# Performance work log

Hardware: AMD Instinct MI355X
Metric: run time of the kernel (lower is better)

The kernel has to match this reference:

```python
import jax, jax.numpy as jnp
import numpy as np

B, N, C, H = 16, 577, 768, 12
KEEP_RATE = 0.7


def setup_inputs() -> dict:
    key = jax.random.key(0)
    k1, k2, k3 = jax.random.split(key, 3)
    x = jax.random.normal(k1, (B, N, C), dtype=jnp.float32)
    W_qkv = jax.random.normal(k2, (C, 3 * C), dtype=jnp.float32) * 0.02
    W_proj = jax.random.normal(k3, (C, C), dtype=jnp.float32) * 0.02
    b_proj = jnp.zeros((C,), dtype=jnp.float32)
    return {"x": x, "W_qkv": W_qkv, "W_proj": W_proj, "b_proj": b_proj}


def reference(x, W_qkv, W_proj, b_proj):
    b, n, c = x.shape
    h = H
    dh = c // h
    scale = dh ** (-0.5)

    # qkv projection -> q,k,v each [B,H,N,dh]
    qkv = (x @ W_qkv).reshape(b, n, 3, h, dh)
    qkv = jnp.transpose(qkv, (2, 0, 3, 1, 4))
    q, k, v = qkv[0], qkv[1], qkv[2]

    # full attention scores [B,H,N,N] (materialized, as in the source)
    attn = jnp.einsum('bhnd,bhmd->bhnm', q, k) * scale

    # --- top_pool from row-0 (CLS) scores, attn_method == 'SUM_ABS_1' ---
    # attn[:, :, 0, :] -> [B,H,N]; sum |.| over heads -> [B,N] (== mean over C=1 channel)
    attn_weight = jnp.sum(jnp.abs(attn[:, :, 0, :]), axis=1)  # [B,N]
    # exclude_first=True: drop CLS, topk over remaining N-1, alpha1=1, alpha2=0 (C==1 -> std=0)
    w = attn_weight[:, 1:]                       # [B, N-1]
    keep_num = max(int((n - 1) * KEEP_RATE), 1)  # static
    _, idx = jax.lax.top_k(w, keep_num)          # [B, keep_num]
    idx = jnp.sort(idx, axis=1)
    idx = jnp.concatenate(
        [jnp.zeros((b, 1), dtype=idx.dtype), idx + 1], axis=1)  # prepend CLS index 0
    # expand to [B, keep_num+1, dim] as in torch (pool dim kwarg == self.dim)
    keep_index = jnp.broadcast_to(idx[:, :, None], (b, keep_num + 1, c))

    # standard attention output
    a = jax.nn.softmax(attn, axis=-1)
    out = jnp.einsum('bhnm,bhmd->bhnd', a, v)    # [B,H,N,dh]
    out = jnp.transpose(out, (0, 2, 1, 3)).reshape(b, n, c)
    out = out @ W_proj + b_proj
    return out, keep_index
```

## Files before the change

kernel.cpp:

```cpp
#include <hip/hip_runtime.h>
#include <hip/hip_bf16.h>
#include <stdint.h>

#define B_    16
#define N_    577
#define C_    768
#define H_    12
#define M_    (B_*N_)
#define QKVN  (3*C_)
#define NKEEP 403
#define KROWS (NKEEP+1)
#define VTLD  640
#define PTLD  72

typedef short s16x8 __attribute__((ext_vector_type(8)));
typedef float f32x4 __attribute__((ext_vector_type(4)));

__device__ __forceinline__ unsigned short f2bf(float x){
  unsigned int u = __float_as_uint(x);
  u += 0x7FFF + ((u >> 16) & 1);
  return (unsigned short)(u >> 16);
}

__device__ __forceinline__ void gld_lds16(const void* g, void* l){
  __builtin_amdgcn_global_load_lds(
      (const __attribute__((address_space(1))) unsigned int*)g,
      (__attribute__((address_space(3))) unsigned int*)l, 16, 0, 0);
}

template<int NT>
__device__ __forceinline__ void tile_map(int L, int& mt, int& nt){
  constexpr int NB = 73*NT;
  int x = L & 7, j = L >> 3;
  if(j < 9*NT){
    nt = j/9; mt = x*9 + (j - nt*9);
  } else {
    mt = 72;
    int offt = 0;
    #pragma unroll
    for(int y=0;y<8;y++) if(y<x) offt += ((NB-1-y)>>3) + 1 - 9*NT;
    nt = offt + (j - 9*NT);
  }
}

__global__ void k_cvt_x(const float* __restrict__ x, unsigned short* __restrict__ xb){
  int i = blockIdx.x*256 + threadIdx.x;
  float4 v = ((const float4*)x)[i];
  ushort4 o; o.x=f2bf(v.x); o.y=f2bf(v.y); o.z=f2bf(v.z); o.w=f2bf(v.w);
  ((ushort4*)xb)[i] = o;
}

__global__ void k_transpose_cvt(const float* __restrict__ in, unsigned short* __restrict__ out,
                                int R, int CC){
  __shared__ float tile[64][65];
  int r0 = blockIdx.y*64, c0 = blockIdx.x*64;
  int tx = threadIdx.x & 63, ty = threadIdx.x >> 6;
  #pragma unroll
  for(int i=0;i<16;i++){
    int r = ty + i*4;
    tile[r][tx] = in[(size_t)(r0+r)*CC + c0 + tx];
  }
  __syncthreads();
  #pragma unroll
  for(int i=0;i<16;i++){
    int c = ty + i*4;
    out[(size_t)(c0+c)*R + r0 + tx] = f2bf(tile[tx][c]);
  }
}

template<int LDC_, bool BF16OUT, bool FUSEV, int NT>
__global__ __launch_bounds__(256) void k_gemm_bt(const unsigned short* __restrict__ A,
                          const unsigned short* __restrict__ Bt,
                          void* __restrict__ Cout,
                          const float* __restrict__ bias, int Mdim,
                          unsigned short* __restrict__ vtbuf){
  __shared__ __align__(16) unsigned short As[128*32];
  __shared__ __align__(16) unsigned short Bs[128*32];
  const int t = threadIdx.x;
  const int w = t>>6, l = t&63, lq = l>>4, lr = l&15;
  const int wm = w>>1, wn = w&1;
  int mt, nt; tile_map<NT>(blockIdx.x, mt, nt);
  const int m0 = mt*128, n0 = nt*128;
  int rA0 = m0 + (t>>2);       if(rA0 >= Mdim) rA0 = Mdim-1;
  int rA1 = m0 + ((t+256)>>2); if(rA1 >= Mdim) rA1 = Mdim-1;
  const unsigned short* gA0 = A  + (size_t)rA0*768 + (t&3)*8;
  const unsigned short* gA1 = A  + (size_t)rA1*768 + (t&3)*8;
  const unsigned short* gB0 = Bt + (size_t)(n0 + (t>>2))*768 + (t&3)*8;
  const unsigned short* gB1 = Bt + (size_t)(n0 + ((t+256)>>2))*768 + (t&3)*8;
  unsigned short* lA0 = As + (size_t)w*512;
  unsigned short* lA1 = As + 2048 + (size_t)w*512;
  unsigned short* lB0 = Bs + (size_t)w*512;
  unsigned short* lB1 = Bs + 2048 + (size_t)w*512;
  f32x4 acc[4][4] = {};
  for(int kt=0; kt<24; ++kt){
    __syncthreads();
    gld_lds16(gA0, lA0); gld_lds16(gA1, lA1);
    gld_lds16(gB0, lB0); gld_lds16(gB1, lB1);
    gA0 += 32; gA1 += 32; gB0 += 32; gB1 += 32;
    __syncthreads();
    s16x8 af[4], bfr[4];
    #pragma unroll
    for(int it=0;it<4;it++) af[it]  = *(const s16x8*)&As[(wm*64+it*16+lr)*32 + lq*8];
    #pragma unroll
    for(int jt=0;jt<4;jt++) bfr[jt] = *(const s16x8*)&Bs[(wn*64+jt*16+lr)*32 + lq*8];
    #pragma unroll
    for(int it=0;it<4;it++)
      #pragma unroll
      for(int jt=0;jt<4;jt++)
        acc[it][jt] = __builtin_amdgcn_mfma_f32_16x16x32_bf16(af[it], bfr[jt], acc[it][jt], 0,0,0);
  }
  if(FUSEV && n0 >= 1536){
    #pragma unroll
    for(int it=0;it<4;it++){
      int tok0 = m0 + wm*64 + it*16 + lq*4;
      #pragma unroll
      for(int jt=0;jt<4;jt++){
        int vrow = (n0 - 1536) + wn*64 + jt*16 + lr;
        ushort4 pk; unsigned short* pks = (unsigned short*)&pk;
        #pragma unroll
        for(int r=0;r<4;r++) pks[r] = f2bf(acc[it][jt][r]);
        int b0 = tok0/577, t0 = tok0 - b0*577;
        if(tok0 + 3 < M_ && t0 + 3 < 577){
          *(ushort4*)&vtbuf[(size_t)(b0*768 + vrow)*VTLD + t0] = pk;
        } else {
          #pragma unroll
          for(int r=0;r<4;r++){
            int tg = tok0 + r;
            if(tg < M_){
              int bb = tg/577, tt = tg - bb*577;
              vtbuf[(size_t)(bb*768 + vrow)*VTLD + tt] = pks[r];
            }
          }
        }
      }
    }
  } else {
    #pragma unroll
    for(int it=0;it<4;it++){
      #pragma unroll
      for(int r=0;r<4;r++){
        int row = m0 + wm*64 + it*16 + lq*4 + r;
        if(row < Mdim){
          #pragma unroll
          for(int jt=0;jt<4;jt++){
            int col = n0 + wn*64 + jt*16 + lr;
            float v = acc[it][jt][r];
            if constexpr (BF16OUT)
              ((unsigned short*)Cout)[(size_t)row*LDC_ + col] = f2bf(v);
            else
              ((float*)Cout)[(size_t)row*LDC_ + col] = v + bias[col];
          }
        }
      }
    }
  }
}

__global__ __launch_bounds__(256,4) void k_attn(const unsigned short* __restrict__ qkv,
                                                const unsigned short* __restrict__ vtbuf,
                                                unsigned short* __restrict__ aout){
  __shared__ __align__(16) unsigned short Ks[64*64];
  __shared__ __align__(16) unsigned short Vt[64*64];
  __shared__ __align__(16) unsigned short Ptt[128*PTLD];
  __shared__ float Ls[4][2][16][4];
  const int blk = blockIdx.x;
  const int bh = blk % 192, qt = blk / 192;
  const int b = bh / 12, h = bh % 12;
  const int t = threadIdx.x, w = t>>6, l = t&63, lq = l>>4, lr = l&15;
  const size_t base = (size_t)(b*577)*2304 + h*64;
  const int q0 = qt*128;
  s16x8 bq[2][2];
  #pragma unroll
  for(int it=0;it<2;it++){
    int qrow = q0 + w*32 + it*16 + lr; if(qrow > 576) qrow = 576;
    #pragma unroll
    for(int ks=0;ks<2;ks++)
      bq[it][ks] = *(const s16x8*)&qkv[base + (size_t)qrow*2304 + ks*32 + lq*8];
  }
  const int srow = w*8 + (l>>3);
  const int cswz8 = (((l&7) ^ (l>>3)) << 3);
  unsigned short* ldsK = Ks + (size_t)w*512;
  unsigned short* ldsV = Vt + (size_t)w*512;
  const unsigned short* gVbase = vtbuf + (size_t)(bh*64)*VTLD + cswz8;

  f32x4 acc_o[2][4] = {};
  float lsum[2] = {0.f, 0.f};
  const float CEXP = 0.18033688011112043f;

  for(int j0=0; j0<577; j0+=64){
    __syncthreads();
    #pragma unroll
    for(int i=0;i<2;i++){
      int krow = j0 + i*32 + srow; if(krow > 576) krow = 576;
      gld_lds16(qkv + base + 768 + (size_t)krow*2304 + cswz8, ldsK + i*2048);
      gld_lds16(gVbase + (size_t)(i*32 + srow)*VTLD + j0,     ldsV + i*2048);
    }
    __syncthreads();
    f32x4 accs[2][4] = {};
    #pragma unroll
    for(int ks=0;ks<2;ks++){
      s16x8 ak[4];
      #pragma unroll
      for(int jt=0;jt<4;jt++){
        int j = jt*16 + lr;
        ak[jt] = *(const s16x8*)&Ks[j*64 + (((4*ks+lq) ^ (j&7))<<3)];
      }
      #pragma unroll
      for(int it=0;it<2;it++)
        #pragma unroll
        for(int jt=0;jt<4;jt++)
          accs[it][jt] = __builtin_amdgcn_mfma_f32_16x16x32_bf16(ak[jt], bq[it][ks], accs[it][jt], 0,0,0);
    }
    #pragma unroll
    for(int it=0;it<2;it++){
      int qlocal = w*32 + it*16 + lr;
      #pragma unroll
      for(int jt=0;jt<4;jt++){
        ushort4 pk;
        unsigned short* pks = (unsigned short*)&pk;
        #pragma unroll
        for(int r=0;r<4;r++){
          int j = j0 + jt*16 + lq*4 + r;
          float p = exp2f(accs[it][jt][r] * CEXP);
          if(j > 576) p = 0.f;
          lsum[it] += p;
          pks[r] = f2bf(p);
        }
        *(ushort4*)&Ptt[qlocal*PTLD + jt*16 + lq*4] = pk;
      }
    }
    #pragma unroll
    for(int ks=0;ks<2;ks++){
      s16x8 ap[2], bv[4];
      #pragma unroll
      for(int it=0;it<2;it++)
        ap[it] = *(const s16x8*)&Ptt[(w*32+it*16+lr)*PTLD + ks*32 + lq*8];
      #pragma unroll
      for(int dt=0;dt<4;dt++){
        int d = dt*16 + lr;
        bv[dt] = *(const s16x8*)&Vt[d*64 + (((4*ks+lq) ^ (d&7))<<3)];
      }
      #pragma unroll
      for(int it=0;it<2;it++)
        #pragma unroll
        for(int dt=0;dt<4;dt++)
          acc_o[it][dt] = __builtin_amdgcn_mfma_f32_16x16x32_bf16(ap[it], bv[dt], acc_o[it][dt], 0,0,0);
    }
  }
  #pragma unroll
  for(int it=0;it<2;it++) Ls[w][it][lr][lq] = lsum[it];
  #pragma unroll
  for(int it=0;it<2;it++){
    #pragma unroll
    for(int r=0;r<4;r++){
      int n = q0 + w*32 + it*16 + lq*4 + r;
      if(n <= 576){
        int q16 = lq*4 + r;
        float lt = Ls[w][it][q16][0] + Ls[w][it][q16][1] + Ls[w][it][q16][2] + Ls[w][it][q16][3];
        float inv = 1.f / lt;
        #pragma unroll
        for(int dt=0;dt<4;dt++)
          aout[(size_t)(b*577+n)*768 + h*64 + dt*16 + lr] = f2bf(acc_o[it][dt][r]*inv);
      }
    }
  }
}

__global__ void k_qcls(const float* __restrict__ x, const float* __restrict__ Wqkv,
                       float* __restrict__ qcls){
  __shared__ float xs[768];
  __shared__ float part[4][64];
  const int b = blockIdx.y, j0 = blockIdx.x*64;
  const int t = threadIdx.x;
  const float* xr = x + (size_t)b*577*768;
  xs[t] = xr[t]; xs[t+256] = xr[t+256]; xs[t+512] = xr[t+512];
  __syncthreads();
  const int jl = t & 63, cs = t >> 6;
  float acc = 0.f;
  const float* wp = Wqkv + (size_t)(cs*192)*2304 + j0 + jl;
  #pragma unroll 4
  for(int c=0;c<192;c++){ acc += xs[cs*192+c] * wp[0]; wp += 2304; }
  part[cs][jl] = acc;
  __syncthreads();
  if(t < 64) qcls[b*768 + j0 + t] = part[0][t]+part[1][t]+part[2][t]+part[3][t];
}
__global__ void k_u(const float* __restrict__ Wqkv, const float* __restrict__ qcls,
                    float* __restrict__ u){
  int h = blockIdx.x, b = blockIdx.y, c = threadIdx.x;
  const float* qc = qcls + b*768 + h*64;
  const float* wr = Wqkv + (size_t)c*2304 + 768 + h*64;
  float acc = 0.f;
  #pragma unroll
  for(int d=0;d<64;d++) acc += wr[d]*qc[d];
  u[(size_t)(b*12+h)*768 + c] = acc;
}
__global__ void k_attw(const float* __restrict__ x, const float* __restrict__ u,
                       float* __restrict__ attw){
  int blk = blockIdx.x;
  int b = blk/577, m = blk%577;
  int lane = threadIdx.x;
  const float* xr = x + (size_t)(b*577+m)*768;
  const float* ub = u + (size_t)b*12*768;
  float part[12];
  #pragma unroll
  for(int h=0;h<12;h++) part[h]=0.f;
  #pragma unroll
  for(int i=0;i<12;i++){
    float xv = xr[i*64 + lane];
    #pragma unroll
    for(int h=0;h<12;h++) part[h] += xv * ub[h*768 + i*64 + lane];
  }
  float s = 0.f;
  #pragma unroll
  for(int h=0;h<12;h++){
    float v = part[h];
    #pragma unroll
    for(int off=32; off; off>>=1) v += __shfl_xor(v, off);
    s += fabsf(v);
  }
  if(lane==0) attw[b*577 + m] = 0.125f * s;
}
__global__ void k_topk(const float* __restrict__ attw, int* __restrict__ idxbuf){
  __shared__ float sw[576];
  __shared__ int wtot[9];
  int b = blockIdx.x, t = threadIdx.x;
  float wv = attw[b*577 + 1 + t];
  sw[t] = wv;
  __syncthreads();
  int rank = 0;
  for(int j=0;j<576;j++){
    float wj = sw[j];
    rank += (wj > wv) || (wj == wv && j < t);
  }
  bool kept = rank < NKEEP;
  unsigned long long mask = __ballot(kept);
  int wid = t>>6, lane = t&63;
  int pos = __popcll(mask & ((1ull<<lane)-1ull));
  if(lane==0) wtot[wid] = __popcll(mask);
  __syncthreads();
  int off0 = 0;
  for(int q=0;q<wid;q++) off0 += wtot[q];
  if(kept) idxbuf[b*KROWS + 1 + off0 + pos] = t+1;
  if(t==0) idxbuf[b*KROWS] = 0;
}
__global__ void k_fill_keep(const int* __restrict__ idxbuf, float* __restrict__ out2){
  int i4 = blockIdx.x*256 + threadIdx.x;
  float v = (float)idxbuf[i4/192];
  ((float4*)out2)[i4] = make_float4(v,v,v,v);
}

extern "C" void kernel_launch(void* const* d_in, const int* in_sizes, int n_in,
                              void* d_out, int out_size, void* d_ws, size_t ws_size,
                              hipStream_t stream){
  const float* x     = (const float*)d_in[0];
  const float* Wqkv  = (const float*)d_in[1];
  const float* Wproj = (const float*)d_in[2];
  const float* bias  = (const float*)d_in[3];
  float* out  = (float*)d_out;
  float* out2 = out + (size_t)M_*768;

  char* ws = (char*)d_ws;
  size_t off = 0;
  auto alloc = [&](size_t bytes)->void*{ void* p = ws + off; off += (bytes + 255) & ~(size_t)255; return p; };
  unsigned short* xb     = (unsigned short*)alloc((size_t)M_*768*2);
  unsigned short* wqkvT  = (unsigned short*)alloc((size_t)QKVN*768*2);
  unsigned short* wprojT = (unsigned short*)alloc((size_t)768*768*2);
  unsigned short* qkvb   = (unsigned short*)alloc((size_t)M_*QKVN*2);
  unsigned short* aoutb  = (unsigned short*)alloc((size_t)M_*768*2);
  unsigned short* vtbuf  = (unsigned short*)alloc((size_t)192*64*VTLD*2);
  float* qcls   = (float*)alloc((size_t)16*768*4);
  float* u      = (float*)alloc((size_t)16*12*768*4);
  float* attw   = (float*)alloc((size_t)16*577*4);
  int*   idxbuf = (int*)alloc((size_t)16*KROWS*4);

  k_cvt_x<<<6924, 256, 0, stream>>>(x, xb);
  k_transpose_cvt<<<dim3(36,12), 256, 0, stream>>>(Wqkv,  wqkvT, 768, 2304);
  k_transpose_cvt<<<dim3(12,12), 256, 0, stream>>>(Wproj, wprojT, 768, 768);
  k_gemm_bt<QKVN, true, true, 18><<<73*18, 256, 0, stream>>>(xb, wqkvT, qkvb, nullptr, M_, vtbuf);
  k_qcls<<<dim3(12,16), 256, 0, stream>>>(x, Wqkv, qcls);
  k_u<<<dim3(12,16), 768, 0, stream>>>(Wqkv, qcls, u);
  k_attw<<<16*577, 64, 0, stream>>>(x, u, attw);
  k_topk<<<16, 576, 0, stream>>>(attw, idxbuf);
  k_fill_keep<<<(16*KROWS*768/4 + 255)/256, 256, 0, stream>>>(idxbuf, out2);
  k_attn<<<960, 256, 0, stream>>>(qkvb, vtbuf, aoutb);
  k_gemm_bt<768, false, false, 6><<<73*6, 256, 0, stream>>>(aoutb, wprojT, out, bias, M_, nullptr);
}
```

Measured before the change: 284.5 us.

## Double-buffer LDS tiles in GEMM and attention to overlap loads with MFMA

Both the bf16 GEMM and the attention kernel now use two LDS stages. The next K-slice (GEMM) or K/V tile (attention) is issued into the alternate buffer before computing on the current one, which also drops one barrier per iteration. The aim is to hide global-to-LDS latency behind MFMA work. The cost is doubled LDS per block: the attention kernel rises to roughly 50 KB, which may cut the number of resident blocks per CU below the four its launch bounds target. Correctness also depends on the async LDS loads having completed before each barrier.

```diff
diff --git a/kernel.cpp b/kernel.cpp
--- a/kernel.cpp
+++ b/kernel.cpp
@@ -74,8 +74,8 @@
                           void* __restrict__ Cout,
                           const float* __restrict__ bias, int Mdim,
                           unsigned short* __restrict__ vtbuf){
-  __shared__ __align__(16) unsigned short As[128*32];
-  __shared__ __align__(16) unsigned short Bs[128*32];
+  __shared__ __align__(16) unsigned short As[2*128*32];
+  __shared__ __align__(16) unsigned short Bs[2*128*32];
   const int t = threadIdx.x;
   const int w = t>>6, l = t&63, lq = l>>4, lr = l&15;
   const int wm = w>>1, wn = w&1;
@@ -87,28 +87,39 @@
   const unsigned short* gA1 = A  + (size_t)rA1*768 + (t&3)*8;
   const unsigned short* gB0 = Bt + (size_t)(n0 + (t>>2))*768 + (t&3)*8;
   const unsigned short* gB1 = Bt + (size_t)(n0 + ((t+256)>>2))*768 + (t&3)*8;
-  unsigned short* lA0 = As + (size_t)w*512;
-  unsigned short* lA1 = As + 2048 + (size_t)w*512;
-  unsigned short* lB0 = Bs + (size_t)w*512;
-  unsigned short* lB1 = Bs + 2048 + (size_t)w*512;
   f32x4 acc[4][4] = {};
-  for(int kt=0; kt<24; ++kt){
-    __syncthreads();
-    gld_lds16(gA0, lA0); gld_lds16(gA1, lA1);
-    gld_lds16(gB0, lB0); gld_lds16(gB1, lB1);
-    gA0 += 32; gA1 += 32; gB0 += 32; gB1 += 32;
-    __syncthreads();
+
+  auto issue = [&](int kt, int s){
+    const int ko = kt*32;
+    unsigned short* a = As + s*4096 + w*512;
+    unsigned short* b = Bs + s*4096 + w*512;
+    gld_lds16(gA0 + ko, a);
+    gld_lds16(gA1 + ko, a + 2048);
+    gld_lds16(gB0 + ko, b);
+    gld_lds16(gB1 + ko, b + 2048);
+  };
+  auto compute = [&](int s){
     s16x8 af[4], bfr[4];
     #pragma unroll
-    for(int it=0;it<4;it++) af[it]  = *(const s16x8*)&As[(wm*64+it*16+lr)*32 + lq*8];
-    #pragma unroll
-    for(int jt=0;jt<4;jt++) bfr[jt] = *(const s16x8*)&Bs[(wn*64+jt*16+lr)*32 + lq*8];
+    for(int it=0;it<4;it++) af[it]  = *(const s16x8*)&As[s*4096 + (wm*64+it*16+lr)*32 + lq*8];
+    #pragma unroll
+    for(int jt=0;jt<4;jt++) bfr[jt] = *(const s16x8*)&Bs[s*4096 + (wn*64+jt*16+lr)*32 + lq*8];
     #pragma unroll
     for(int it=0;it<4;it++)
       #pragma unroll
       for(int jt=0;jt<4;jt++)
         acc[it][jt] = __builtin_amdgcn_mfma_f32_16x16x32_bf16(af[it], bfr[jt], acc[it][jt], 0,0,0);
-  }
+  };
+
+  issue(0, 0);
+  for(int kt=1; kt<24; ++kt){
+    __syncthreads();
+    issue(kt, kt&1);
+    compute((kt-1)&1);
+  }
+  __syncthreads();
+  compute(1);
+
   if(FUSEV && n0 >= 1536){
     #pragma unroll
     for(int it=0;it<4;it++){
@@ -159,8 +170,8 @@
 __global__ __launch_bounds__(256,4) void k_attn(const unsigned short* __restrict__ qkv,
                                                 const unsigned short* __restrict__ vtbuf,
                                                 unsigned short* __restrict__ aout){
-  __shared__ __align__(16) unsigned short Ks[64*64];
-  __shared__ __align__(16) unsigned short Vt[64*64];
+  __shared__ __align__(16) unsigned short Ks[2*64*64];
+  __shared__ __align__(16) unsigned short Vt[2*64*64];
   __shared__ __align__(16) unsigned short Ptt[128*PTLD];
   __shared__ float Ls[4][2][16][4];
   const int blk = blockIdx.x;
@@ -179,23 +190,26 @@
   }
   const int srow = w*8 + (l>>3);
   const int cswz8 = (((l&7) ^ (l>>3)) << 3);
-  unsigned short* ldsK = Ks + (size_t)w*512;
-  unsigned short* ldsV = Vt + (size_t)w*512;
   const unsigned short* gVbase = vtbuf + (size_t)(bh*64)*VTLD + cswz8;
 
   f32x4 acc_o[2][4] = {};
   float lsum[2] = {0.f, 0.f};
   const float CEXP = 0.18033688011112043f;
 
-  for(int j0=0; j0<577; j0+=64){
-    __syncthreads();
+  auto issueKV = [&](int j0, int s){
     #pragma unroll
     for(int i=0;i<2;i++){
       int krow = j0 + i*32 + srow; if(krow > 576) krow = 576;
-      gld_lds16(qkv + base + 768 + (size_t)krow*2304 + cswz8, ldsK + i*2048);
-      gld_lds16(gVbase + (size_t)(i*32 + srow)*VTLD + j0,     ldsV + i*2048);
-    }
+      gld_lds16(qkv + base + 768 + (size_t)krow*2304 + cswz8, Ks + s*4096 + w*512 + i*2048);
+      gld_lds16(gVbase + (size_t)(i*32 + srow)*VTLD + j0,     Vt + s*4096 + w*512 + i*2048);
+    }
+  };
+
+  issueKV(0, 0);
+  for(int jt5=0; jt5<10; ++jt5){
+    const int j0 = jt5*64, s = jt5&1;
     __syncthreads();
+    if(jt5 < 9) issueKV(j0+64, s^1);
     f32x4 accs[2][4] = {};
     #pragma unroll
     for(int ks=0;ks<2;ks++){
@@ -203,7 +217,7 @@
       #pragma unroll
       for(int jt=0;jt<4;jt++){
         int j = jt*16 + lr;
-        ak[jt] = *(const s16x8*)&Ks[j*64 + (((4*ks+lq) ^ (j&7))<<3)];
+        ak[jt] = *(const s16x8*)&Ks[s*4096 + j*64 + (((4*ks+lq) ^ (j&7))<<3)];
       }
       #pragma unroll
       for(int it=0;it<2;it++)
@@ -238,7 +252,7 @@
       #pragma unroll
       for(int dt=0;dt<4;dt++){
         int d = dt*16 + lr;
-        bv[dt] = *(const s16x8*)&Vt[d*64 + (((4*ks+lq) ^ (d&7))<<3)];
+        bv[dt] = *(const s16x8*)&Vt[s*4096 + d*64 + (((4*ks+lq) ^ (d&7))<<3)];
       }
       #pragma unroll
       for(int it=0;it<2;it++)
```

Result: slower. 296.3 us (+4.2%).

## Use 64-row tiles for output projection and peel attention edge tile

Applied to the files above, without the earlier changes.

Adds a separate projection GEMM kernel with 64x128 tiles, so it launches 870 blocks instead of 438 and fills more compute units. The tile mapping is generalized to handle the last M tiles. The attention key loop is split into full tiles plus one masked edge tile, which removes the per-element bounds check from the main loop. GEMM addressing now uses a per-iteration offset instead of pointer increments. Smaller tiles raise the B-matrix reload traffic.

```diff
diff --git a/kernel.cpp b/kernel.cpp
--- a/kernel.cpp
+++ b/kernel.cpp
@@ -28,18 +28,19 @@
       (__attribute__((address_space(3))) unsigned int*)l, 16, 0, 0);
 }
 
-template<int NT>
+template<int NT, int M9, int MTILES>
 __device__ __forceinline__ void tile_map(int L, int& mt, int& nt){
-  constexpr int NB = 73*NT;
+  constexpr int NB = MTILES*NT;
   int x = L & 7, j = L >> 3;
-  if(j < 9*NT){
-    nt = j/9; mt = x*9 + (j - nt*9);
+  if(j < M9*NT){
+    nt = j/M9; mt = x*M9 + (j - nt*M9);
   } else {
-    mt = 72;
     int offt = 0;
     #pragma unroll
-    for(int y=0;y<8;y++) if(y<x) offt += ((NB-1-y)>>3) + 1 - 9*NT;
-    nt = offt + (j - 9*NT);
+    for(int y=0;y<8;y++) if(y<x) offt += ((NB-1-y)>>3) + 1 - M9*NT;
+    int ft = offt + (j - M9*NT);
+    mt = 8*M9 + ft/NT;
+    nt = ft - (ft/NT)*NT;
   }
 }
 
@@ -79,7 +80,7 @@
   const int t = threadIdx.x;
   const int w = t>>6, l = t&63, lq = l>>4, lr = l&15;
   const int wm = w>>1, wn = w&1;
-  int mt, nt; tile_map<NT>(blockIdx.x, mt, nt);
+  int mt, nt; tile_map<NT, 9, 73>(blockIdx.x, mt, nt);
   const int m0 = mt*128, n0 = nt*128;
   int rA0 = m0 + (t>>2);       if(rA0 >= Mdim) rA0 = Mdim-1;
   int rA1 = m0 + ((t+256)>>2); if(rA1 >= Mdim) rA1 = Mdim-1;
@@ -93,10 +94,10 @@
   unsigned short* lB1 = Bs + 2048 + (size_t)w*512;
   f32x4 acc[4][4] = {};
   for(int kt=0; kt<24; ++kt){
-    __syncthreads();
-    gld_lds16(gA0, lA0); gld_lds16(gA1, lA1);
-    gld_lds16(gB0, lB0); gld_lds16(gB1, lB1);
-    gA0 += 32; gA1 += 32; gB0 += 32; gB1 += 32;
+    const int ko = kt*32;
+    __syncthreads();
+    gld_lds16(gA0 + ko, lA0); gld_lds16(gA1 + ko, lA1);
+    gld_lds16(gB0 + ko, lB0); gld_lds16(gB1 + ko, lB1);
     __syncthreads();
     s16x8 af[4], bfr[4];
     #pragma unroll
@@ -156,6 +157,58 @@
   }
 }
 
+__global__ __launch_bounds__(256) void k_gemm_bt64(const unsigned short* __restrict__ A,
+                          const unsigned short* __restrict__ Bt,
+                          float* __restrict__ Cout,
+                          const float* __restrict__ bias, int Mdim){
+  __shared__ __align__(16) unsigned short As[64*32];
+  __shared__ __align__(16) unsigned short Bs[128*32];
+  const int t = threadIdx.x;
+  const int w = t>>6, l = t&63, lq = l>>4, lr = l&15;
+  const int wm = w>>1, wn = w&1;
+  int mt, nt; tile_map<6, 18, 145>(blockIdx.x, mt, nt);
+  const int m0 = mt*64, n0 = nt*128;
+  int rA0 = m0 + (t>>2);       if(rA0 >= Mdim) rA0 = Mdim-1;
+  const unsigned short* gA0 = A  + (size_t)rA0*768 + (t&3)*8;
+  const unsigned short* gB0 = Bt + (size_t)(n0 + (t>>2))*768 + (t&3)*8;
+  const unsigned short* gB1 = Bt + (size_t)(n0 + ((t+256)>>2))*768 + (t&3)*8;
+  unsigned short* lA0 = As + (size_t)w*512;
+  unsigned short* lB0 = Bs + (size_t)w*512;
+  unsigned short* lB1 = Bs + 2048 + (size_t)w*512;
+  f32x4 acc[2][4] = {};
+  for(int kt=0; kt<24; ++kt){
+    const int ko = kt*32;
+    __syncthreads();
+    gld_lds16(gA0 + ko, lA0);
+    gld_lds16(gB0 + ko, lB0); gld_lds16(gB1 + ko, lB1);
+    __syncthreads();
+    s16x8 af[2], bfr[4];
+    #pragma unroll
+    for(int it=0;it<2;it++) af[it]  = *(const s16x8*)&As[(wm*32+it*16+lr)*32 + lq*8];
+    #pragma unroll
+    for(int jt=0;jt<4;jt++) bfr[jt] = *(const s16x8*)&Bs[(wn*64+jt*16+lr)*32 + lq*8];
+    #pragma unroll
+    for(int it=0;it<2;it++)
+      #pragma unroll
+      for(int jt=0;jt<4;jt++)
+        acc[it][jt] = __builtin_amdgcn_mfma_f32_16x16x32_bf16(af[it], bfr[jt], acc[it][jt], 0,0,0);
+  }
+  #pragma unroll
+  for(int it=0;it<2;it++){
+    #pragma unroll
+    for(int r=0;r<4;r++){
+      int row = m0 + wm*32 + it*16 + lq*4 + r;
+      if(row < Mdim){
+        #pragma unroll
+        for(int jt=0;jt<4;jt++){
+          int col = n0 + wn*64 + jt*16 + lr;
+          Cout[(size_t)row*768 + col] = acc[it][jt][r] + bias[col];
+        }
+      }
+    }
+  }
+}
+
 __global__ __launch_bounds__(256,4) void k_attn(const unsigned short* __restrict__ qkv,
                                                 const unsigned short* __restrict__ vtbuf,
                                                 unsigned short* __restrict__ aout){
@@ -187,7 +240,7 @@
   float lsum[2] = {0.f, 0.f};
   const float CEXP = 0.18033688011112043f;
 
-  for(int j0=0; j0<577; j0+=64){
+  auto tile_body = [&](int j0, bool edge){
     __syncthreads();
     #pragma unroll
     for(int i=0;i<2;i++){
@@ -220,9 +273,8 @@
         unsigned short* pks = (unsigned short*)&pk;
         #pragma unroll
         for(int r=0;r<4;r++){
-          int j = j0 + jt*16 + lq*4 + r;
           float p = exp2f(accs[it][jt][r] * CEXP);
-          if(j > 576) p = 0.f;
+          if(edge){ if(j0 + jt*16 + lq*4 + r > 576) p = 0.f; }
           lsum[it] += p;
           pks[r] = f2bf(p);
         }
@@ -246,7 +298,10 @@
         for(int dt=0;dt<4;dt++)
           acc_o[it][dt] = __builtin_amdgcn_mfma_f32_16x16x32_bf16(ap[it], bv[dt], acc_o[it][dt], 0,0,0);
     }
-  }
+  };
+  for(int j0=0; j0<576; j0+=64) tile_body(j0, false);
+  tile_body(576, true);
+
   #pragma unroll
   for(int it=0;it<2;it++) Ls[w][it][lr][lq] = lsum[it];
   #pragma unroll
@@ -383,5 +438,5 @@
   k_topk<<<16, 576, 0, stream>>>(attw, idxbuf);
   k_fill_keep<<<(16*KROWS*768/4 + 255)/256, 256, 0, stream>>>(idxbuf, out2);
   k_attn<<<960, 256, 0, stream>>>(qkvb, vtbuf, aoutb);
-  k_gemm_bt<768, false, false, 6><<<73*6, 256, 0, stream>>>(aoutb, wprojT, out, bias, M_, nullptr);
-}
+  k_gemm_bt64<<<145*6, 256, 0, stream>>>(aoutb, wprojT, out, bias, M_);
+}
```

New measurement: 282.5 us. No clear change (-0.7%).
